# Kernel tuning notes

Hardware: AMD Instinct MI355X
Metric: run time of the kernel (lower is better)

The kernel has to match this reference:

```python
import jax, jax.numpy as jnp
import numpy as np

F = 26          # number of sparse fields
V = 100000      # vocab per field
D = 32          # embedding dim
DENSE = 13
HID = (1024, 512, 256)
B = 16384


def setup_inputs() -> dict:
    key = jax.random.key(0)
    ks = jax.random.split(key, 16)
    x_sparse = jax.random.randint(ks[0], (B, F), 0, V, dtype=jnp.int32)
    x_dense = jax.random.normal(ks[1], (B, DENSE), dtype=jnp.float32)
    emb_tables = jax.random.normal(ks[2], (F, V, D), dtype=jnp.float32) * 0.05
    lin_tables = jax.random.normal(ks[3], (F, V), dtype=jnp.float32) * 0.05
    dnn_in = F * D + DENSE
    dims = (dnn_in,) + HID
    params = {}
    for i in range(len(HID)):
        params[f'W{i}'] = jax.random.normal(ks[4 + i], (dims[i], dims[i + 1]), dtype=jnp.float32) * (1.0 / np.sqrt(dims[i]))
        params[f'b{i}'] = jnp.zeros((dims[i + 1],), dtype=jnp.float32)
    Wout = jax.random.normal(ks[10], (HID[-1], 1), dtype=jnp.float32) * (1.0 / np.sqrt(HID[-1]))
    bout = jnp.zeros((1,), dtype=jnp.float32)
    return dict(x_sparse=x_sparse, x_dense=x_dense, emb_tables=emb_tables,
                lin_tables=lin_tables,
                W0=params['W0'], b0=params['b0'],
                W1=params['W1'], b1=params['b1'],
                W2=params['W2'], b2=params['b2'],
                Wout=Wout, bout=bout)


def reference(x_sparse, x_dense, emb_tables, lin_tables,
              W0, b0, W1, b1, W2, b2, Wout, bout):
    f_idx = jnp.arange(F)[None, :]            # [1, F]
    # batched multi-field gather: [B, F, D] and [B, F]
    emb = emb_tables[f_idx, x_sparse]          # [B, F, D]
    lin = lin_tables[f_idx, x_sparse]          # [B, F]
    linear_logit = lin.sum(axis=1)             # [B]
    # FM pairwise sum_{i<j} <e_i, e_j> via sum-square identity
    s = emb.sum(axis=1)                        # [B, D]
    fm_logit = 0.5 * ((s * s).sum(axis=-1) - (emb * emb).sum(axis=(1, 2)))  # [B]
    # DNN on concatenated embeddings + dense feats
    h = jnp.concatenate([emb.reshape(emb.shape[0], F * D), x_dense], axis=1)
    h = jax.nn.relu(h @ W0 + b0)
    h = jax.nn.relu(h @ W1 + b1)
    h = jax.nn.relu(h @ W2 + b2)
    dnn_logit = (h @ Wout + bout)[:, 0]        # [B]
    return jax.nn.sigmoid(linear_logit + fm_logit + dnn_logit)
```

## Files before the change

kernel.cpp:

```cpp
#include <hip/hip_runtime.h>
#include <math.h>


typedef __attribute__((ext_vector_type(8))) short shortx8;
typedef __attribute__((ext_vector_type(4))) float floatx4;

#define AS1 __attribute__((address_space(1)))
#define AS3 __attribute__((address_space(3)))

__device__ __forceinline__ void load_lds_16(const void* g, void* l) {
    __builtin_amdgcn_global_load_lds((AS1 void*)g, (AS3 void*)l, 16, 0, 0);
}

__device__ __forceinline__ unsigned short f2bf(float x) {
    union { float f; unsigned int u; } v; v.f = x;
    unsigned int r = v.u + 0x7fffu + ((v.u >> 16) & 1u);
    return (unsigned short)(r >> 16);
}

__global__ void wtrans(const float* __restrict__ W, unsigned short* __restrict__ Wt,
                       int K, int N, int Kpad)
{
    __shared__ float tile[32][33];
    const int k0 = blockIdx.x * 32, n0 = blockIdx.y * 32;
    const int tx = threadIdx.x, ty = threadIdx.y;
#pragma unroll
    for (int i = 0; i < 32; i += 8) {
        int k = k0 + ty + i;
        tile[ty + i][tx] = (k < K) ? W[(size_t)k * N + (n0 + tx)] : 0.f;
    }
    __syncthreads();
#pragma unroll
    for (int i = 0; i < 32; i += 8) {
        int n = n0 + ty + i, kk = k0 + tx;
        Wt[(size_t)n * Kpad + kk] = f2bf(tile[tx][ty + i]);
    }
}

__global__ __launch_bounds__(256)
void gather_fm(const int* __restrict__ xs, const float* __restrict__ xd,
               const float* __restrict__ emb, const float* __restrict__ lint,
               unsigned short* __restrict__ h0, float* __restrict__ lg)
{
    const int lane = threadIdx.x & 63;
    const int wave = threadIdx.x >> 6;
    const int b = blockIdx.x * 4 + wave;

    int idx = 0; float linv = 0.f;
    if (lane < 26) {
        idx = xs[b * 26 + lane];
        linv = lint[(size_t)lane * 100000 + idx];
    }
    const int d = lane & 31;
    const int half = lane >> 5;
    float s = 0.f, sq = 0.f;
    unsigned short* hrow = h0 + (size_t)b * 864;
#pragma unroll
    for (int it = 0; it < 13; ++it) {
        int f = it * 2 + half;
        int fidx = __shfl(idx, f);
        float v = emb[((size_t)f * 100000 + (size_t)fidx) * 32 + d];
        s += v; sq += v * v;
        hrow[f * 32 + d] = f2bf(v);
    }
    s += __shfl_xor(s, 32);
    float t = 0.25f * s * s - 0.5f * sq + linv;
#pragma unroll
    for (int off = 32; off >= 1; off >>= 1) t += __shfl_xor(t, off);
    if (lane == 0) lg[b] = t;

    if (lane < 13) {
        hrow[832 + lane] = f2bf(xd[b * 13 + lane]);
    } else if (lane < 32) {
        hrow[832 + lane] = 0;
    }
}

template <typename OUT_T>
__global__ __launch_bounds__(256)
void gemm_bias_relu(const unsigned short* __restrict__ X,
                    const unsigned short* __restrict__ Wt,
                    const float* __restrict__ bias,
                    OUT_T* __restrict__ Y,
                    int M, int N, int K)
{
    __shared__ alignas(16) unsigned short As[128 * 32];
    __shared__ alignas(16) unsigned short Bs[128 * 32];

    const int tid  = threadIdx.x;
    const int lane = tid & 63;
    const int wave = tid >> 6;
    const int bm = blockIdx.x * 128;
    const int bn = blockIdx.y * 128;
    const int wm = (wave & 1) * 64;
    const int wn = (wave >> 1) * 64;
    const int lrow  = lane & 15;
    const int lquad = lane >> 4;

    floatx4 acc[4][4];
    const floatx4 z4 = {0.f, 0.f, 0.f, 0.f};
#pragma unroll
    for (int i = 0; i < 4; ++i)
#pragma unroll
        for (int j = 0; j < 4; ++j) acc[i][j] = z4;

    const int r0 = tid >> 2,        kp0 = (tid & 3) << 3;
    const int r1 = (tid + 256) >> 2, kp1 = ((tid + 256) & 3) << 3;

    for (int k0 = 0; k0 < K; k0 += 32) {
        load_lds_16(X  + (size_t)(bm + r0) * K + (k0 + kp0), As + (size_t)tid * 8);
        load_lds_16(Wt + (size_t)(bn + r0) * K + (k0 + kp0), Bs + (size_t)tid * 8);
        load_lds_16(X  + (size_t)(bm + r1) * K + (k0 + kp1), As + (size_t)(tid + 256) * 8);
        load_lds_16(Wt + (size_t)(bn + r1) * K + (k0 + kp1), Bs + (size_t)(tid + 256) * 8);
        __syncthreads();

        shortx8 a[4], b[4];
#pragma unroll
        for (int i = 0; i < 4; ++i)
            a[i] = *(const shortx8*)(As + (wm + i * 16 + lrow) * 32 + lquad * 8);
#pragma unroll
        for (int j = 0; j < 4; ++j)
            b[j] = *(const shortx8*)(Bs + (wn + j * 16 + lrow) * 32 + lquad * 8);
#pragma unroll
        for (int i = 0; i < 4; ++i)
#pragma unroll
            for (int j = 0; j < 4; ++j)
                acc[i][j] = __builtin_amdgcn_mfma_f32_16x16x32_bf16(a[i], b[j], acc[i][j], 0, 0, 0);
        __syncthreads();
    }

#pragma unroll
    for (int i = 0; i < 4; ++i) {
        const int row = bm + wm + i * 16 + lquad * 4;
#pragma unroll
        for (int j = 0; j < 4; ++j) {
            const int col = bn + wn + j * 16 + lrow;
            const float bv = bias[col];
#pragma unroll
            for (int r = 0; r < 4; ++r) {
                float v = fmaxf(acc[i][j][r] + bv, 0.f);
                size_t off = (size_t)(row + r) * N + col;
                if (sizeof(OUT_T) == 4) ((float*)Y)[off] = v;
                else                    ((unsigned short*)Y)[off] = f2bf(v);
            }
        }
    }
}

__global__ __launch_bounds__(256)
void final_out(const float* __restrict__ h3, const float* __restrict__ Wo,
               const float* __restrict__ bo, const float* __restrict__ lg,
               float* __restrict__ out)
{
    const int lane = threadIdx.x & 63;
    const int wave = threadIdx.x >> 6;
    const int b = blockIdx.x * 4 + wave;
    const float* row = h3 + (size_t)b * 256;
    float acc = 0.f;
#pragma unroll
    for (int q = 0; q < 4; ++q) acc += row[lane + q * 64] * Wo[lane + q * 64];
#pragma unroll
    for (int off = 32; off >= 1; off >>= 1) acc += __shfl_xor(acc, off);
    if (lane == 0) {
        float x = acc + bo[0] + lg[b];
        out[b] = 1.f / (1.f + expf(-x));
    }
}

extern "C" void kernel_launch(void* const* d_in, const int* in_sizes, int n_in,
                              void* d_out, int out_size, void* d_ws, size_t ws_size,
                              hipStream_t stream)
{
    const int*   xs = (const int*)d_in[0];
    const float* xd = (const float*)d_in[1];
    const float* em = (const float*)d_in[2];
    const float* li = (const float*)d_in[3];
    const float* W0 = (const float*)d_in[4];
    const float* b0 = (const float*)d_in[5];
    const float* W1 = (const float*)d_in[6];
    const float* b1 = (const float*)d_in[7];
    const float* W2 = (const float*)d_in[8];
    const float* b2 = (const float*)d_in[9];
    const float* Wo = (const float*)d_in[10];
    const float* bo = (const float*)d_in[11];
    float* out = (float*)d_out;

    char* ws = (char*)d_ws;
    unsigned short* h0  = (unsigned short*)(ws);
    unsigned short* h1  = (unsigned short*)(ws + 28311552);
    unsigned short* h2  = (unsigned short*)(ws);
    float*          h3  = (float*)(ws + 28311552);
    unsigned short* Wt0 = (unsigned short*)(ws + 61865984);
    unsigned short* Wt1 = (unsigned short*)(ws + 63635456);
    unsigned short* Wt2 = (unsigned short*)(ws + 64684032);
    float*          lg  = (float*)(ws + 64946176);

    dim3 tb(32, 8);
    wtrans<<<dim3(27, 32), tb, 0, stream>>>(W0, Wt0, 845, 1024, 864);
    wtrans<<<dim3(32, 16), tb, 0, stream>>>(W1, Wt1, 1024, 512, 1024);
    wtrans<<<dim3(16, 8),  tb, 0, stream>>>(W2, Wt2, 512, 256, 512);

    gather_fm<<<4096, 256, 0, stream>>>(xs, xd, em, li, h0, lg);

    gemm_bias_relu<unsigned short><<<dim3(128, 8), 256, 0, stream>>>(h0, Wt0, b0, h1, 16384, 1024, 864);
    gemm_bias_relu<unsigned short><<<dim3(128, 4), 256, 0, stream>>>(h1, Wt1, b1, h2, 16384, 512, 1024);
    gemm_bias_relu<float>         <<<dim3(128, 2), 256, 0, stream>>>(h2, Wt2, b2, h3, 16384, 256, 512);

    final_out<<<4096, 256, 0, stream>>>(h3, Wo, bo, lg, out);
}
```

Baseline: 517.6 us.

## Fuse last GEMM with output head and widen first GEMM tile to 256 columns

Fuses the third GEMM (512->256) with the final dot product, bias, linear/FM logits and sigmoid. The 256-wide fp32 h3 activation is reduced in registers and LDS instead of being written to and re-read from global memory, which also removes one launch. The first GEMM now uses a 128x256 tile so each A tile is reused across twice as many columns, at the cost of more accumulator registers (launch bounds 256,2). The fused kernel uses only 256 blocks of 64 rows each, which may underfill the GPU.

```diff
diff --git a/kernel.cpp b/kernel.cpp
--- a/kernel.cpp
+++ b/kernel.cpp
@@ -76,12 +76,80 @@
     }
 }
 
-template <typename OUT_T>
+__global__ __launch_bounds__(256, 2)
+void gemm_bign(const unsigned short* __restrict__ X,
+               const unsigned short* __restrict__ Wt,
+               const float* __restrict__ bias,
+               unsigned short* __restrict__ Y,
+               int M, int N, int K)
+{
+    __shared__ alignas(16) unsigned short As[128 * 32];
+    __shared__ alignas(16) unsigned short Bs[256 * 32];
+
+    const int tid  = threadIdx.x;
+    const int lane = tid & 63;
+    const int wave = tid >> 6;
+    const int bm = blockIdx.x * 128;
+    const int bn = blockIdx.y * 256;
+    const int wm = (wave & 1) * 64;
+    const int wn = (wave >> 1) * 128;
+    const int lrow  = lane & 15;
+    const int lquad = lane >> 4;
+
+    floatx4 acc[4][8];
+    const floatx4 z4 = {0.f, 0.f, 0.f, 0.f};
+#pragma unroll
+    for (int i = 0; i < 4; ++i)
+#pragma unroll
+        for (int j = 0; j < 8; ++j) acc[i][j] = z4;
+
+    const int ar = tid >> 2, akp = (tid & 3) << 3;
+
+    for (int k0 = 0; k0 < K; k0 += 32) {
+        load_lds_16(X + (size_t)(bm + ar) * K + (k0 + akp), As + (size_t)tid * 8);
+        load_lds_16(X + (size_t)(bm + ar + 64) * K + (k0 + akp), As + (size_t)(tid + 256) * 8);
+#pragma unroll
+        for (int q = 0; q < 4; ++q) {
+            int c = tid + q * 256;
+            load_lds_16(Wt + (size_t)(bn + (c >> 2)) * K + (k0 + akp), Bs + (size_t)c * 8);
+        }
+        __syncthreads();
+
+        shortx8 a[4];
+#pragma unroll
+        for (int i = 0; i < 4; ++i)
+            a[i] = *(const shortx8*)(As + (wm + i * 16 + lrow) * 32 + lquad * 8);
+#pragma unroll
+        for (int j = 0; j < 8; ++j) {
+            shortx8 b = *(const shortx8*)(Bs + (wn + j * 16 + lrow) * 32 + lquad * 8);
+#pragma unroll
+            for (int i = 0; i < 4; ++i)
+                acc[i][j] = __builtin_amdgcn_mfma_f32_16x16x32_bf16(a[i], b, acc[i][j], 0, 0, 0);
+        }
+        __syncthreads();
+    }
+
+#pragma unroll
+    for (int i = 0; i < 4; ++i) {
+        const int row = bm + wm + i * 16 + lquad * 4;
+#pragma unroll
+        for (int j = 0; j < 8; ++j) {
+            const int col = bn + wn + j * 16 + lrow;
+            const float bv = bias[col];
+#pragma unroll
+            for (int r = 0; r < 4; ++r) {
+                float v = fmaxf(acc[i][j][r] + bv, 0.f);
+                Y[(size_t)(row + r) * N + col] = f2bf(v);
+            }
+        }
+    }
+}
+
 __global__ __launch_bounds__(256)
 void gemm_bias_relu(const unsigned short* __restrict__ X,
                     const unsigned short* __restrict__ Wt,
                     const float* __restrict__ bias,
-                    OUT_T* __restrict__ Y,
+                    unsigned short* __restrict__ Y,
                     int M, int N, int K)
 {
     __shared__ alignas(16) unsigned short As[128 * 32];
@@ -104,14 +172,13 @@
 #pragma unroll
         for (int j = 0; j < 4; ++j) acc[i][j] = z4;
 
-    const int r0 = tid >> 2,        kp0 = (tid & 3) << 3;
-    const int r1 = (tid + 256) >> 2, kp1 = ((tid + 256) & 3) << 3;
+    const int r0 = tid >> 2, kp0 = (tid & 3) << 3;
 
     for (int k0 = 0; k0 < K; k0 += 32) {
         load_lds_16(X  + (size_t)(bm + r0) * K + (k0 + kp0), As + (size_t)tid * 8);
         load_lds_16(Wt + (size_t)(bn + r0) * K + (k0 + kp0), Bs + (size_t)tid * 8);
-        load_lds_16(X  + (size_t)(bm + r1) * K + (k0 + kp1), As + (size_t)(tid + 256) * 8);
-        load_lds_16(Wt + (size_t)(bn + r1) * K + (k0 + kp1), Bs + (size_t)(tid + 256) * 8);
+        load_lds_16(X  + (size_t)(bm + r0 + 64) * K + (k0 + kp0), As + (size_t)(tid + 256) * 8);
+        load_lds_16(Wt + (size_t)(bn + r0 + 64) * K + (k0 + kp0), Bs + (size_t)(tid + 256) * 8);
         __syncthreads();
 
         shortx8 a[4], b[4];
@@ -139,31 +206,96 @@
 #pragma unroll
             for (int r = 0; r < 4; ++r) {
                 float v = fmaxf(acc[i][j][r] + bv, 0.f);
-                size_t off = (size_t)(row + r) * N + col;
-                if (sizeof(OUT_T) == 4) ((float*)Y)[off] = v;
-                else                    ((unsigned short*)Y)[off] = f2bf(v);
+                Y[(size_t)(row + r) * N + col] = f2bf(v);
             }
         }
     }
 }
 
 __global__ __launch_bounds__(256)
-void final_out(const float* __restrict__ h3, const float* __restrict__ Wo,
-               const float* __restrict__ bo, const float* __restrict__ lg,
-               float* __restrict__ out)
-{
-    const int lane = threadIdx.x & 63;
-    const int wave = threadIdx.x >> 6;
-    const int b = blockIdx.x * 4 + wave;
-    const float* row = h3 + (size_t)b * 256;
-    float acc = 0.f;
-#pragma unroll
-    for (int q = 0; q < 4; ++q) acc += row[lane + q * 64] * Wo[lane + q * 64];
-#pragma unroll
-    for (int off = 32; off >= 1; off >>= 1) acc += __shfl_xor(acc, off);
-    if (lane == 0) {
-        float x = acc + bo[0] + lg[b];
-        out[b] = 1.f / (1.f + expf(-x));
+void gemm3_final(const unsigned short* __restrict__ X,
+                 const unsigned short* __restrict__ Wt,
+                 const float* __restrict__ bias,
+                 const float* __restrict__ Wo,
+                 const float* __restrict__ bo,
+                 const float* __restrict__ lg,
+                 float* __restrict__ out)
+{
+    const int K = 512;
+    __shared__ alignas(16) unsigned short As[64 * 32];
+    __shared__ alignas(16) unsigned short Bs[256 * 32];
+    __shared__ float red[4][64];
+
+    const int tid  = threadIdx.x;
+    const int lane = tid & 63;
+    const int wave = tid >> 6;
+    const int bm = blockIdx.x * 64;
+    const int wn = wave * 64;
+    const int lrow  = lane & 15;
+    const int lquad = lane >> 4;
+
+    floatx4 acc[4][4];
+    const floatx4 z4 = {0.f, 0.f, 0.f, 0.f};
+#pragma unroll
+    for (int i = 0; i < 4; ++i)
+#pragma unroll
+        for (int j = 0; j < 4; ++j) acc[i][j] = z4;
+
+    const int ar = tid >> 2, akp = (tid & 3) << 3;
+
+    for (int k0 = 0; k0 < K; k0 += 32) {
+        load_lds_16(X + (size_t)(bm + ar) * K + (k0 + akp), As + (size_t)tid * 8);
+#pragma unroll
+        for (int q = 0; q < 4; ++q) {
+            int c = tid + q * 256;
+            load_lds_16(Wt + (size_t)(c >> 2) * K + (k0 + akp), Bs + (size_t)c * 8);
+        }
+        __syncthreads();
+
+        shortx8 a[4], b[4];
+#pragma unroll
+        for (int i = 0; i < 4; ++i)
+            a[i] = *(const shortx8*)(As + (i * 16 + lrow) * 32 + lquad * 8);
+#pragma unroll
+        for (int j = 0; j < 4; ++j)
+            b[j] = *(const shortx8*)(Bs + (wn + j * 16 + lrow) * 32 + lquad * 8);
+#pragma unroll
+        for (int i = 0; i < 4; ++i)
+#pragma unroll
+            for (int j = 0; j < 4; ++j)
+                acc[i][j] = __builtin_amdgcn_mfma_f32_16x16x32_bf16(a[i], b[j], acc[i][j], 0, 0, 0);
+        __syncthreads();
+    }
+
+    float bv[4], wv[4];
+#pragma unroll
+    for (int j = 0; j < 4; ++j) {
+        int col = wn + j * 16 + lrow;
+        bv[j] = bias[col];
+        wv[j] = Wo[col];
+    }
+#pragma unroll
+    for (int i = 0; i < 4; ++i) {
+#pragma unroll
+        for (int r = 0; r < 4; ++r) {
+            float p = 0.f;
+#pragma unroll
+            for (int j = 0; j < 4; ++j) {
+                float v = fmaxf(acc[i][j][r] + bv[j], 0.f);
+                p += v * wv[j];
+            }
+            p += __shfl_xor(p, 1);
+            p += __shfl_xor(p, 2);
+            p += __shfl_xor(p, 4);
+            p += __shfl_xor(p, 8);
+            if (lrow == 0) red[wave][i * 16 + lquad * 4 + r] = p;
+        }
+    }
+    __syncthreads();
+    if (tid < 64) {
+        float s = red[0][tid] + red[1][tid] + red[2][tid] + red[3][tid];
+        float x = s + bo[0] + lg[bm + tid];
+        out[bm + tid] = 1.f / (1.f + expf(-x));
     }
 }
 
@@ -189,7 +321,6 @@
     unsigned short* h0  = (unsigned short*)(ws);
     unsigned short* h1  = (unsigned short*)(ws + 28311552);
     unsigned short* h2  = (unsigned short*)(ws);
-    float*          h3  = (float*)(ws + 28311552);
     unsigned short* Wt0 = (unsigned short*)(ws + 61865984);
     unsigned short* Wt1 = (unsigned short*)(ws + 63635456);
     unsigned short* Wt2 = (unsigned short*)(ws + 64684032);
@@ -202,9 +333,7 @@
 
     gather_fm<<<4096, 256, 0, stream>>>(xs, xd, em, li, h0, lg);
 
-    gemm_bias_relu<unsigned short><<<dim3(128, 8), 256, 0, stream>>>(h0, Wt0, b0, h1, 16384, 1024, 864);
-    gemm_bias_relu<unsigned short><<<dim3(128, 4), 256, 0, stream>>>(h1, Wt1, b1, h2, 16384, 512, 1024);
-    gemm_bias_relu<float>         <<<dim3(128, 2), 256, 0, stream>>>(h2, Wt2, b2, h3, 16384, 256, 512);
-
-    final_out<<<4096, 256, 0, stream>>>(h3, Wo, bo, lg, out);
-}
+    gemm_bign<<<dim3(128, 4), 256, 0, stream>>>(h0, Wt0, b0, h1, 16384, 1024, 864);
+    gemm_bias_relu<<<dim3(128, 4), 256, 0, stream>>>(h1, Wt1, b1, h2, 16384, 512, 1024);
+    gemm3_final<<<256, 256, 0, stream>>>(h2, Wt2, b2, Wo, bo, lg, out);
+}
```

New measurement: 499.2 us. -3.5%, faster.
